# Optimization experiments

Measured on AMD Instinct MI355X. Metric: run time of the kernel, lower is better.

## Reference

```python
import jax, jax.numpy as jnp
import numpy as np

WS = 8          # window size
DIM = 192
NH = 6          # num heads
HD = DIM // NH  # head dim = 32
HIDDEN = 768    # mlp_ratio 4
EPS = 1e-5


def _rel_tables(ws):
    # continuous relative-coords table, shape (1, 2w-1, 2w-1, 2)
    r = np.arange(-(ws - 1), ws, dtype=np.float32)
    table = np.stack(np.meshgrid(r, r, indexing='ij'), axis=-1)[None]
    table = table / (ws - 1) * 8.0
    # relative position index, shape (N, N)
    coords = np.stack(np.meshgrid(np.arange(ws), np.arange(ws), indexing='ij'))
    cf = coords.reshape(2, -1)
    rel = (cf[:, :, None] - cf[:, None, :]).transpose(1, 2, 0).astype(np.int64)
    rel[:, :, 0] += ws - 1
    rel[:, :, 1] += ws - 1
    rel[:, :, 0] *= 2 * ws - 1
    idx = rel.sum(-1)
    return jnp.asarray(table), jnp.asarray(idx)

_TABLE, _RPI = _rel_tables(WS)


def _layernorm(x, g, b):
    m = jnp.mean(x, -1, keepdims=True)
    v = jnp.var(x, -1, keepdims=True)
    return (x - m) * jax.lax.rsqrt(v + EPS) * g + b


def setup_inputs() -> dict:
    key = jax.random.key(0)
    ks = jax.random.split(key, 12)
    B, H, W = 2, 256, 256
    s = 0.02
    return {
        'x': jax.random.normal(ks[0], (B, H * W, DIM), jnp.float32),
        'scale': jax.random.uniform(ks[1], (1, 2), jnp.float32, 0.5, 2.0),
        'norm1_g': jnp.ones((DIM,), jnp.float32),
        'norm1_b': jnp.zeros((DIM,), jnp.float32),
        'qkv_w': jax.random.normal(ks[2], (DIM, 3 * DIM), jnp.float32) * s,
        'qkv_b': jnp.zeros((3 * DIM,), jnp.float32),
        'proj_w': jax.random.normal(ks[3], (DIM, DIM), jnp.float32) * s,
        'proj_b': jnp.zeros((DIM,), jnp.float32),
        'cpb_w1': jax.random.normal(ks[4], (4, 512), jnp.float32) * s,
        'cpb_b1': jnp.zeros((512,), jnp.float32),
        'cpb_w2': jax.random.normal(ks[5], (512, NH), jnp.float32) * s,
        'cpb_b2': jnp.zeros((NH,), jnp.float32),
        'norm2_g': jnp.ones((DIM,), jnp.float32),
        'norm2_b': jnp.zeros((DIM,), jnp.float32),
        'fc1_w': jax.random.normal(ks[6], (DIM, HIDDEN), jnp.float32) * s,
        'fc1_b': jnp.zeros((HIDDEN,), jnp.float32),
        'fc2_w': jax.random.normal(ks[7], (HIDDEN, DIM), jnp.float32) * s,
        'fc2_b': jnp.zeros((DIM,), jnp.float32),
        'dw_w': jax.random.normal(ks[8], (HIDDEN, 1, 3, 3), jnp.float32) * s,
        'dw_b': jnp.zeros((HIDDEN,), jnp.float32),
        'H': 256,
        'W': 256,
    }


def reference(x, scale, norm1_g, norm1_b, qkv_w, qkv_b, proj_w, proj_b,
              cpb_w1, cpb_b1, cpb_w2, cpb_b2, norm2_g, norm2_b,
              fc1_w, fc1_b, fc2_w, fc2_b, dw_w, dw_b, H, W):
    B, L, C = x.shape
    N = WS * WS
    shortcut = x

    # ---- W-MSA branch ----
    h = _layernorm(x, norm1_g, norm1_b).reshape(B, H, W, C)
    # window partition -> (B*nW, N, C)
    h = h.reshape(B, H // WS, WS, W // WS, WS, C).transpose(0, 1, 3, 2, 4, 5)
    xw = h.reshape(-1, N, C)
    B_ = xw.shape[0]

    qkv = (xw @ qkv_w + qkv_b).reshape(B_, N, 3, NH, HD).transpose(2, 0, 3, 1, 4)
    q, k, v = qkv[0], qkv[1], qkv[2]          # (B_, NH, N, HD)
    q = q * (HD ** -0.5)
    attn = jnp.einsum('bhnd,bhmd->bhnm', q, k)  # (B_, NH, N, N)

    # continuous relative position bias from cpb MLP conditioned on `scale`
    rel_cell = jnp.broadcast_to(scale[:, None, None, :], _TABLE.shape)  # (1,2w-1,2w-1,2)
    coords4 = jnp.concatenate([_TABLE, rel_cell], axis=-1)              # (1,2w-1,2w-1,4)
    bias_tab = (jax.nn.relu(coords4 @ cpb_w1 + cpb_b1) @ cpb_w2 + cpb_b2).reshape(-1, NH)
    rpb = bias_tab[_RPI.reshape(-1)].reshape(N, N, NH).transpose(2, 0, 1)  # (NH,N,N)
    attn = jax.nn.softmax(attn + rpb[None], axis=-1)

    out = jnp.einsum('bhnm,bhmd->bhnd', attn, v).transpose(0, 2, 1, 3).reshape(B_, N, C)
    out = out @ proj_w + proj_b

    # window reverse
    out = out.reshape(B, H // WS, W // WS, WS, WS, C).transpose(0, 1, 3, 2, 4, 5)
    out = out.reshape(B, L, C)
    x = shortcut + out

    # ---- conv-augmented MLP branch ----
    h = _layernorm(x, norm2_g, norm2_b)
    h = jax.nn.gelu(h @ fc1_w + fc1_b, approximate=False)   # (B, L, HIDDEN)
    hc = h.transpose(0, 2, 1).reshape(B, HIDDEN, H, W)
    hc = jax.lax.conv_general_dilated(
        hc, dw_w, window_strides=(1, 1), padding=((1, 1), (1, 1)),
        dimension_numbers=('NCHW', 'OIHW', 'NCHW'), feature_group_count=HIDDEN)
    hc = hc + dw_b[None, :, None, None]
    h = hc.reshape(B, HIDDEN, L).transpose(0, 2, 1)
    h = jax.nn.gelu(h, approximate=False)
    h = h @ fc2_w + fc2_b
    return x + h
```

## Files before the change

### kernel.cpp

```cpp
#include <hip/hip_runtime.h>
#include <hip/hip_bf16.h>

typedef __attribute__((ext_vector_type(8))) short  bf16x8;
typedef __attribute__((ext_vector_type(4))) float  f32x4;
typedef __attribute__((ext_vector_type(8))) unsigned short u16x8;
typedef __attribute__((ext_vector_type(4))) unsigned short u16x4;

__device__ __forceinline__ unsigned short f2b(float f) {
    unsigned int u = __builtin_bit_cast(unsigned int, f);
    u += 0x7FFFu + ((u >> 16) & 1u);
    return (unsigned short)(u >> 16);
}
__device__ __forceinline__ float b2f(unsigned short u) {
    return __builtin_bit_cast(float, (unsigned int)u << 16);
}
__device__ __forceinline__ float gelu_fast(float x) {
    float d = 1.0f + __expf(-1.702f * x);
    return x * __builtin_amdgcn_rcpf(d);
}
__device__ __forceinline__ int wperm(int m) {
    int w = m >> 6, n = m & 63;
    int b = w >> 10, wy = (w >> 5) & 31, wx = w & 31;
    int y = wy * 8 + (n >> 3), xx = wx * 8 + (n & 7);
    return (b << 16) + (y << 8) + xx;
}

__device__ __forceinline__ void gload_lds16(const void* g, void* l) {
    __builtin_amdgcn_global_load_lds(
        (const __attribute__((address_space(1))) void*)g,
        (__attribute__((address_space(3))) void*)l, 16, 0, 0);
}

__global__ void transpose_w(const float* __restrict__ in, unsigned short* __restrict__ out,
                            int K, int N) {
    int i = blockIdx.x * 256 + threadIdx.x;
    if (i >= K * N) return;
    int n = i / K, k = i - n * K;
    out[i] = f2b(in[k * N + n]);
}

__global__ void transpose_wf(const float* __restrict__ in, float* __restrict__ out,
                             int K, int N) {
    int i = blockIdx.x * 256 + threadIdx.x;
    if (i >= K * N) return;
    int n = i / K, k = i - n * K;
    out[i] = in[k * N + n];
}

__global__ __launch_bounds__(256) void cpb_kernel(
    const float* __restrict__ scale, const float* __restrict__ w1, const float* __restrict__ b1,
    const float* __restrict__ w2, const float* __restrict__ b2, float* __restrict__ btab) {
    int t = threadIdx.x;
    if (t >= 225) return;
    int i = t / 15, j = t - (t / 15) * 15;
    float ti = (i - 7) * (8.0f / 7.0f);
    float tj = (j - 7) * (8.0f / 7.0f);
    float s0 = scale[0], s1 = scale[1];
    float acc[6];
    #pragma unroll
    for (int h = 0; h < 6; ++h) acc[h] = b2[h];
    for (int k = 0; k < 512; ++k) {
        float hv = ti * w1[k] + tj * w1[512 + k] + s0 * w1[1024 + k] + s1 * w1[1536 + k] + b1[k];
        hv = fmaxf(hv, 0.f);
        #pragma unroll
        for (int h = 0; h < 6; ++h) acc[h] += hv * w2[k * 6 + h];
    }
    #pragma unroll
    for (int h = 0; h < 6; ++h) btab[t * 6 + h] = acc[h];
}

template<int MODE>
__global__ __launch_bounds__(512) void gemm64(
    const float* __restrict__ Af,
    const float* __restrict__ lng, const float* __restrict__ lnb,
    const unsigned short* __restrict__ Bt, const float* __restrict__ bias,
    unsigned short* __restrict__ oq, unsigned short* __restrict__ ok2, unsigned short* __restrict__ ov) {
    constexpr int NCT = 3;
    __shared__ __align__(16) unsigned short Asw[3 * 64 * 64];
    __shared__ __align__(16) unsigned short Bsw[2 * 192 * 64];
    const int t = threadIdx.x, lane = t & 63, wv8 = t >> 6;
    const int wm = wv8 >> 2, wn = wv8 & 3;
    const int l15 = lane & 15, lq = lane >> 4;
    const int m0 = blockIdx.x * 64;

    int boffs[3];
    #pragma unroll
    for (int s = 0; s < 3; ++s) {
        int row = (wv8 + 8 * s) * 8 + (lane >> 3);
        boffs[s] = row * 192 + ((lane & 7) ^ (lane >> 3)) * 8;
    }
    #pragma unroll
    for (int s = 0; s < 3; ++s)
        gload_lds16(Bt + boffs[s], (char*)Bsw + (wv8 + 8 * s) * 1024);

    {
        int row = t >> 3, oct = t & 7;
        const float* p = Af + (size_t)wperm(m0 + row) * 192 + oct * 24;
        f32x4 v[6];
        float s = 0.f, q = 0.f;
        #pragma unroll
        for (int i = 0; i < 6; ++i) {
            v[i] = *(const f32x4*)(p + i * 4);
            #pragma unroll
            for (int j = 0; j < 4; ++j) { s += v[i][j]; q += v[i][j] * v[i][j]; }
        }
        s += __shfl_xor(s, 1); s += __shfl_xor(s, 2); s += __shfl_xor(s, 4);
        q += __shfl_xor(q, 1); q += __shfl_xor(q, 2); q += __shfl_xor(q, 4);
        float mean = s * (1.f / 192.f);
        float rstd = rsqrtf(q * (1.f / 192.f) - mean * mean + 1e-5f);
        #pragma unroll
        for (int i = 0; i < 6; ++i) {
            int k = oct * 24 + i * 4;
            u16x4 pk;
            #pragma unroll
            for (int j = 0; j < 4; ++j)
                pk[j] = f2b((v[i][j] - mean) * rstd * lng[k + j] + lnb[k + j]);
            int cc = k >> 6, ch = (k >> 2) & 15;
            int byte = cc * 8192 + row * 128 +
                       ((((ch >> 1) ^ (row & 7)) << 4) + ((ch & 1) << 3));
            *(u16x4*)((char*)Asw + byte) = pk;
        }
        asm volatile("s_waitcnt lgkmcnt(0)" ::: "memory");
    }

    const int axor = (l15 & 7) << 4;
    int cur = 0, it = 0;
    for (int ct = 0; ct < NCT; ++ct) {
        f32x4 acc[2][3];
        #pragma unroll
        for (int i = 0; i < 2; ++i)
            #pragma unroll
            for (int j = 0; j < 3; ++j) acc[i][j] = (f32x4){0.f, 0.f, 0.f, 0.f};
        for (int c = 0; c < 3; ++c, ++it) {
            if (it < NCT * 3 - 1) {
                int ctn = (c == 2) ? ct + 1 : ct;
                int cn  = (c == 2) ? 0 : c + 1;
                #pragma unroll
                for (int s = 0; s < 3; ++s)
                    gload_lds16(Bt + (size_t)ctn * 36864 + boffs[s] + cn * 64,
                                (char*)Bsw + (cur ^ 1) * 24576 + (wv8 + 8 * s) * 1024);
                asm volatile("s_waitcnt vmcnt(3)" ::: "memory");
            } else {
                asm volatile("s_waitcnt vmcnt(0)" ::: "memory");
            }
            __builtin_amdgcn_sched_barrier(0);
            __builtin_amdgcn_s_barrier();
            __builtin_amdgcn_sched_barrier(0);
            const char* Al = (const char*)Asw + c * 8192;
            const char* Bl = (const char*)Bsw + cur * 24576;
            #pragma unroll
            for (int kk = 0; kk < 2; ++kk) {
                bf16x8 a[2], bb[3];
                #pragma unroll
                for (int mt = 0; mt < 2; ++mt)
                    a[mt] = *(const bf16x8*)(Al + (wm * 32 + mt * 16 + l15) * 128 +
                                             ((kk << 6) ^ (lq << 4) ^ axor));
                #pragma unroll
                for (int nt = 0; nt < 3; ++nt)
                    bb[nt] = *(const bf16x8*)(Bl + (wn * 48 + nt * 16 + l15) * 128 +
                                              ((kk << 6) ^ (lq << 4) ^ axor));
                #pragma unroll
                for (int mt = 0; mt < 2; ++mt)
                    #pragma unroll
                    for (int nt = 0; nt < 3; ++nt)
                        acc[mt][nt] = __builtin_amdgcn_mfma_f32_16x16x32_bf16(a[mt], bb[nt], acc[mt][nt], 0, 0, 0);
            }
            __builtin_amdgcn_sched_barrier(0);
            __builtin_amdgcn_s_barrier();
            cur ^= 1;
        }
        unsigned short* dst = (ct == 0) ? oq : (ct == 1) ? ok2 : ov;
        float qs = (ct == 0) ? 0.17677669529663689f : 1.0f;
        #pragma unroll
        for (int mt = 0; mt < 2; ++mt)
            #pragma unroll
            for (int nt = 0; nt < 3; ++nt)
                #pragma unroll
                for (int r = 0; r < 4; ++r) {
                    int m = m0 + wm * 32 + mt * 16 + lq * 4 + r;
                    int col = wn * 48 + nt * 16 + l15;
                    float v = (acc[mt][nt][r] + bias[ct * 192 + col]) * qs;
                    int head = col >> 5, d = col & 31;
                    int w = m >> 6, n = m & 63;
                    dst[((size_t)(w * 6 + head) * 64 + n) * 32 + d] = f2b(v);
                }
    }
}

__global__ __launch_bounds__(512) void attn_proj_fc1(
    const unsigned short* __restrict__ qb, const unsigned short* __restrict__ kb,
    const unsigned short* __restrict__ vb, const float* __restrict__ btab,
    const float* __restrict__ resid,
    const unsigned short* __restrict__ projT, const float* __restrict__ projb,
    const unsigned short* __restrict__ fc1T, const float* __restrict__ fc1b,
    const float* __restrict__ n2g, const float* __restrict__ n2b,
    float* __restrict__ ofp, unsigned short* __restrict__ obf) {
    __shared__ __align__(16) unsigned short Asw[3 * 64 * 64];
    __shared__ __align__(16) unsigned short Bsw[2 * 192 * 64];
    __shared__ float scratch[1352];
    const int t = threadIdx.x, lane = t & 63, wv8 = t >> 6;
    const int wm = wv8 >> 2, wn = wv8 & 3;
    const int l15 = lane & 15, lq = lane >> 4;
    const int win = blockIdx.x;
    const int m0 = win * 64;
    const int axor = (l15 & 7) << 4;

    for (int i = t; i < 1350; i += 512) {
        int h = i / 225, idx = i - h * 225;
        scratch[i] = btab[idx * 6 + h];
    }
    __syncthreads();

    f32x4 o[4][2];
    if (wv8 < 6) {
        const size_t bid = (size_t)(win * 6 + wv8);
        const unsigned short* qp = qb + bid * 2048;
        const unsigned short* kp = kb + bid * 2048;
        const unsigned short* vp = vb + bid * 2048;
        bf16x8 qf[4], kf[4];
        #pragma unroll
        for (int i = 0; i < 4; ++i) {
            qf[i] = *(const bf16x8*)(qp + (i * 16 + l15) * 32 + lq * 8);
            kf[i] = *(const bf16x8*)(kp + (i * 16 + l15) * 32 + lq * 8);
        }
        #pragma unroll
        for (int i = 0; i < 4; ++i) {
            int c = lane + i * 64;
            int mr = c >> 2, d0 = (c & 3) * 8;
            u16x8 v = *(const u16x8*)(vp + mr * 32 + d0);
            #pragma unroll
            for (int j = 0; j < 8; ++j) {
                int row = d0 + j;
                int byte = wv8 * 4096 + row * 128 +
                           (((mr >> 3) ^ (row & 7)) << 4) + (mr & 7) * 2;
                *(unsigned short*)((char*)Asw + byte) = v[j];
            }
        }
        #pragma unroll
        for (int mt = 0; mt < 4; ++mt) {
            f32x4 s[4];
            #pragma unroll
            for (int nt = 0; nt < 4; ++nt)
                s[nt] = __builtin_amdgcn_mfma_f32_16x16x32_bf16(
                    qf[mt], kf[nt], (f32x4){0.f, 0.f, 0.f, 0.f}, 0, 0, 0);
            #pragma unroll
            for (int r = 0; r < 4; ++r) {
                int n = mt * 16 + lq * 4 + r;
                int ny = n >> 3, nx = n & 7;
                float sv[4];
                float mx = -1e30f;
                #pragma unroll
                for (int nt = 0; nt < 4; ++nt) {
                    int m = nt * 16 + l15;
                    int idx = (ny - (m >> 3) + 7) * 15 + (nx - (m & 7) + 7);
                    float val = s[nt][r] + scratch[wv8 * 225 + idx];
                    sv[nt] = val;
                    mx = fmaxf(mx, val);
                }
                #pragma unroll
                for (int off = 1; off < 16; off <<= 1) mx = fmaxf(mx, __shfl_xor(mx, off));
                float sum = 0.f;
                #pragma unroll
                for (int nt = 0; nt < 4; ++nt) { sv[nt] = __expf(sv[nt] - mx); sum += sv[nt]; }
                #pragma unroll
                for (int off = 1; off < 16; off <<= 1) sum += __shfl_xor(sum, off);
                float inv = 1.f / sum;
                #pragma unroll
                for (int nt = 0; nt < 4; ++nt) {
                    int col = nt * 16 + l15;
                    int byte = wv8 * 8192 + n * 128 +
                               (((col >> 3) ^ (n & 7)) << 4) + (col & 7) * 2;
                    *(unsigned short*)((char*)Bsw + byte) = f2b(sv[nt] * inv);
                }
            }
        }
        asm volatile("s_waitcnt lgkmcnt(0)" ::: "memory");
        #pragma unroll
        for (int i = 0; i < 4; ++i)
            #pragma unroll
            for (int j = 0; j < 2; ++j) o[i][j] = (f32x4){0.f, 0.f, 0.f, 0.f};
        #pragma unroll
        for (int mt = 0; mt < 4; ++mt)
            #pragma unroll
            for (int kk = 0; kk < 2; ++kk) {
                bf16x8 a = *(const bf16x8*)((char*)Bsw + wv8 * 8192 +
                    (mt * 16 + l15) * 128 + ((kk << 6) ^ (lq << 4) ^ axor));
                #pragma unroll
                for (int dt = 0; dt < 2; ++dt) {
                    bf16x8 b = *(const bf16x8*)((char*)Asw + wv8 * 4096 +
                        (dt * 16 + l15) * 128 + ((kk << 6) ^ (lq << 4) ^ axor));
                    o[mt][dt] = __builtin_amdgcn_mfma_f32_16x16x32_bf16(a, b, o[mt][dt], 0, 0, 0);
                }
            }
    }
    __syncthreads();
    if (wv8 < 6) {
        #pragma unroll
        for (int mt = 0; mt < 4; ++mt)
            #pragma unroll
            for (int dt = 0; dt < 2; ++dt)
                #pragma unroll
                for (int r = 0; r < 4; ++r) {
                    int row = mt * 16 + lq * 4 + r;
                    int k = wv8 * 32 + dt * 16 + l15;
                    int cc = k >> 6, k6 = k & 63;
                    int byte = cc * 8192 + row * 128 +
                               (((k6 >> 3) ^ (row & 7)) << 4) + (k6 & 7) * 2;
                    *(unsigned short*)((char*)Asw + byte) = f2b(o[mt][dt][r]);
                }
    }
    int boffs[3];
    #pragma unroll
    for (int s = 0; s < 3; ++s) {
        int row = (wv8 + 8 * s) * 8 + (lane >> 3);
        boffs[s] = row * 192 + ((lane & 7) ^ (lane >> 3)) * 8;
    }
    #pragma unroll
    for (int s = 0; s < 3; ++s)
        gload_lds16(projT + boffs[s], (char*)Bsw + (wv8 + 8 * s) * 1024);
    __syncthreads();

    int cur = 0;
    f32x4 acc[2][3];
    #pragma unroll
    for (int i = 0; i < 2; ++i)
        #pragma unroll
        for (int j = 0; j < 3; ++j) acc[i][j] = (f32x4){0.f, 0.f, 0.f, 0.f};
    for (int c = 0; c < 3; ++c) {
        if (c < 2) {
            #pragma unroll
            for (int s = 0; s < 3; ++s)
                gload_lds16(projT + boffs[s] + (c + 1) * 64,
                            (char*)Bsw + (cur ^ 1) * 24576 + (wv8 + 8 * s) * 1024);
        } else {
            #pragma unroll
            for (int s = 0; s < 3; ++s)
                gload_lds16(fc1T + boffs[s],
                            (char*)Bsw + (cur ^ 1) * 24576 + (wv8 + 8 * s) * 1024);
        }
        asm volatile("s_waitcnt vmcnt(3)" ::: "memory");
        __builtin_amdgcn_sched_barrier(0);
        __builtin_amdgcn_s_barrier();
        __builtin_amdgcn_sched_barrier(0);
        const char* Al = (const char*)Asw + c * 8192;
        const char* Bl = (const char*)Bsw + cur * 24576;
        #pragma unroll
        for (int kk = 0; kk < 2; ++kk) {
            bf16x8 a[2], bb[3];
            #pragma unroll
            for (int mt = 0; mt < 2; ++mt)
                a[mt] = *(const bf16x8*)(Al + (wm * 32 + mt * 16 + l15) * 128 +
                                         ((kk << 6) ^ (lq << 4) ^ axor));
            #pragma unroll
            for (int nt = 0; nt < 3; ++nt)
                bb[nt] = *(const bf16x8*)(Bl + (wn * 48 + nt * 16 + l15) * 128 +
                                          ((kk << 6) ^ (lq << 4) ^ axor));
            #pragma unroll
            for (int mt = 0; mt < 2; ++mt)
                #pragma unroll
                for (int nt = 0; nt < 3; ++nt)
                    acc[mt][nt] = __builtin_amdgcn_mfma_f32_16x16x32_bf16(a[mt], bb[nt], acc[mt][nt], 0, 0, 0);
        }
        __builtin_amdgcn_sched_barrier(0);
        __builtin_amdgcn_s_barrier();
        cur ^= 1;
    }
    float* sred = scratch;
    float* srow = scratch + 512;
    float hw[2][3][4];
    #pragma unroll
    for (int mt = 0; mt < 2; ++mt) {
        #pragma unroll
        for (int r = 0; r < 4; ++r) {
            int row = wm * 32 + mt * 16 + lq * 4 + r;
            int r2 = wperm(m0 + row);
            float s = 0.f, q = 0.f;
            #pragma unroll
            for (int nt = 0; nt < 3; ++nt) {
                int col = wn * 48 + nt * 16 + l15;
                size_t idx = (size_t)r2 * 192 + col;
                float wv = resid[idx] + acc[mt][nt][r] + projb[col];
                ofp[idx] = wv;
                hw[mt][nt][r] = wv;
                s += wv;
                q += wv * wv;
            }
            #pragma unroll
            for (int off = 1; off < 16; off <<= 1) {
                s += __shfl_xor(s, off);
                q += __shfl_xor(q, off);
            }
            if (l15 == 0) {
                sred[row * 8 + wn * 2]     = s;
                sred[row * 8 + wn * 2 + 1] = q;
            }
        }
    }
    __syncthreads();
    if (t < 64) {
        float s = sred[t * 8] + sred[t * 8 + 2] + sred[t * 8 + 4] + sred[t * 8 + 6];
        float q = sred[t * 8 + 1] + sred[t * 8 + 3] + sred[t * 8 + 5] + sred[t * 8 + 7];
        float mean = s * (1.f / 192.f);
        float var = q * (1.f / 192.f) - mean * mean;
        srow[t * 2] = mean;
        srow[t * 2 + 1] = rsqrtf(var + 1e-5f);
    }
    __syncthreads();
    {
        float g3[3], b3[3];
        #pragma unroll
        for (int nt = 0; nt < 3; ++nt) {
            int col = wn * 48 + nt * 16 + l15;
            g3[nt] = n2g[col];
            b3[nt] = n2b[col];
        }
        #pragma unroll
        for (int mt = 0; mt < 2; ++mt)
            #pragma unroll
            for (int r = 0; r < 4; ++r) {
                int row = wm * 32 + mt * 16 + lq * 4 + r;
                float mean = srow[row * 2], rstd = srow[row * 2 + 1];
                #pragma unroll
                for (int nt = 0; nt < 3; ++nt) {
                    int k = wn * 48 + nt * 16 + l15;
                    float nv = (hw[mt][nt][r] - mean) * rstd * g3[nt] + b3[nt];
                    int cc = k >> 6, k6 = k & 63;
                    int byte = cc * 8192 + row * 128 +
                               (((k6 >> 3) ^ (row & 7)) << 4) + (k6 & 7) * 2;
                    *(unsigned short*)((char*)Asw + byte) = f2b(nv);
                }
            }
    }
    __syncthreads();

    for (int ct = 0; ct < 4; ++ct) {
        f32x4 a2[2][3];
        #pragma unroll
        for (int i = 0; i < 2; ++i)
            #pragma unroll
            for (int j = 0; j < 3; ++j) a2[i][j] = (f32x4){0.f, 0.f, 0.f, 0.f};
        for (int c = 0; c < 3; ++c) {
            int it = ct * 3 + c;
            if (it < 11) {
                int ctn = (c == 2) ? ct + 1 : ct;
                int cn  = (c == 2) ? 0 : c + 1;
                #pragma unroll
                for (int s = 0; s < 3; ++s)
                    gload_lds16(fc1T + (size_t)ctn * 36864 + boffs[s] + cn * 64,
                                (char*)Bsw + (cur ^ 1) * 24576 + (wv8 + 8 * s) * 1024);
                asm volatile("s_waitcnt vmcnt(3)" ::: "memory");
            } else {
                asm volatile("s_waitcnt vmcnt(0)" ::: "memory");
            }
            __builtin_amdgcn_sched_barrier(0);
            __builtin_amdgcn_s_barrier();
            __builtin_amdgcn_sched_barrier(0);
            const char* Al = (const char*)Asw + c * 8192;
            const char* Bl = (const char*)Bsw + cur * 24576;
            #pragma unroll
            for (int kk = 0; kk < 2; ++kk) {
                bf16x8 a[2], bb[3];
                #pragma unroll
                for (int mt = 0; mt < 2; ++mt)
                    a[mt] = *(const bf16x8*)(Al + (wm * 32 + mt * 16 + l15) * 128 +
                                             ((kk << 6) ^ (lq << 4) ^ axor));
                #pragma unroll
                for (int nt = 0; nt < 3; ++nt)
                    bb[nt] = *(const bf16x8*)(Bl + (wn * 48 + nt * 16 + l15) * 128 +
                                              ((kk << 6) ^ (lq << 4) ^ axor));
                #pragma unroll
                for (int mt = 0; mt < 2; ++mt)
                    #pragma unroll
                    for (int nt = 0; nt < 3; ++nt)
                        a2[mt][nt] = __builtin_amdgcn_mfma_f32_16x16x32_bf16(a[mt], bb[nt], a2[mt][nt], 0, 0, 0);
            }
            __builtin_amdgcn_sched_barrier(0);
            __builtin_amdgcn_s_barrier();
            cur ^= 1;
        }
        #pragma unroll
        for (int mt = 0; mt < 2; ++mt)
            #pragma unroll
            for (int nt = 0; nt < 3; ++nt)
                #pragma unroll
                for (int r = 0; r < 4; ++r) {
                    int m = m0 + wm * 32 + mt * 16 + lq * 4 + r;
                    int col = wn * 48 + nt * 16 + l15;
                    obf[(size_t)wperm(m) * 768 + ct * 192 + col] =
                        f2b(gelu_fast(a2[mt][nt][r] + fc1b[ct * 192 + col]));
                }
    }
}

__global__ __launch_bounds__(512) void conv_fc2_v14(
    const unsigned short* __restrict__ m1, const float* __restrict__ dwwTf,
    const float* __restrict__ dwb, const unsigned short* __restrict__ fc2T,
    const float* __restrict__ fc2b, float* __restrict__ out) {
    __shared__ __align__(16) unsigned short Xs[26 * 512];
    __shared__ __align__(16) unsigned short As[128 * 72];
    __shared__ __align__(16) unsigned short Bsw[192 * 64];
    const int t = threadIdx.x;
    const int g = ((blockIdx.x & 7) << 7) + (blockIdx.x >> 3);
    const int b = g >> 9, yt = (g >> 3) & 63, xq = g & 7;
    const int y0 = yt * 4, x0 = xq * 32;
    const int cg = t & 7, lx = t >> 3;
    const int xx = lx & 31, yy0 = lx >> 5;
    const size_t ibase = (size_t)b * 65536;

    const int lane = t & 63, wv8 = t >> 6;
    const int wm = wv8 >> 1, wn = wv8 & 1;
    const int l15 = lane & 15, lq = lane >> 4;

    int xoff[4];
    #pragma unroll
    for (int s = 0; s < 4; ++s) {
        int seg = wv8 + 8 * s;
        int e = seg * 512 + lane * 8;
        e = min(e, 13048);
        int row = e / 2176;
        int rem = e - row * 2176;
        int px = rem >> 6, ch = rem & 63;
        int gy = min(max(y0 - 1 + row, 0), 255);
        int gx = min(max(x0 - 1 + px, 0), 255);
        xoff[s] = ((b << 16) + (gy << 8) + gx) * 768 + ch;
    }
    int boff[3];
    #pragma unroll
    for (int s = 0; s < 3; ++s) {
        int row = (wv8 + 8 * s) * 8 + (lane >> 3);
        boff[s] = row * 768 + ((lane & 7) ^ (lane >> 3)) * 8;
    }

    f32x4 acc[2][6];
    #pragma unroll
    for (int i = 0; i < 2; ++i)
        #pragma unroll
        for (int j = 0; j < 6; ++j) acc[i][j] = (f32x4){0.f, 0.f, 0.f, 0.f};

    #pragma unroll
    for (int s = 0; s < 4; ++s)
        if (wv8 + 8 * s < 26)
            gload_lds16(m1 + xoff[s], (char*)Xs + (wv8 + 8 * s) * 1024);
    #pragma unroll
    for (int s = 0; s < 3; ++s)
        gload_lds16(fc2T + boff[s], (char*)Bsw + (wv8 + 8 * s) * 1024);

    const int xb = xx * 128 + cg * 16;
    const int gxp = x0 + xx;
    const bool xok0 = gxp >= 1;
    const bool xok2 = gxp <= 254;
    const int oy0 = y0 + yy0;
    const int o00 = (lq * 16) ^ ((l15 & 7) << 4);
    const int brow = (wn * 96 + l15) * 128;

    for (int k0 = 0; k0 < 768; k0 += 64) {
        const int c0 = k0 + cg * 8;
        asm volatile("s_waitcnt vmcnt(0)" ::: "memory");
        __syncthreads();
        float a0[8], a1[8];
        #pragma unroll
        for (int j = 0; j < 8; ++j) { a0[j] = 0.f; a1[j] = 0.f; }
        #pragma unroll
        for (int kx = 0; kx < 3; ++kx) {
            if (kx == 0 && !xok0) continue;
            if (kx == 2 && !xok2) continue;
            #pragma unroll
            for (int ky = 0; ky < 3; ++ky) {
                const float* wp = dwwTf + (ky * 3 + kx) * 768 + c0;
                f32x4 w0 = *(const f32x4*)wp;
                f32x4 w1 = *(const f32x4*)(wp + 4);
                if ((unsigned)(oy0 + ky - 1) < 256u) {
                    u16x8 in = *(const u16x8*)((const char*)Xs +
                        (yy0 + ky) * 4352 + xb + kx * 128);
                    #pragma unroll
                    for (int j = 0; j < 4; ++j) {
                        a0[j]     += b2f(in[j]) * w0[j];
                        a0[4 + j] += b2f(in[4 + j]) * w1[j];
                    }
                }
                if ((unsigned)(oy0 + ky + 1) < 256u) {
                    u16x8 in = *(const u16x8*)((const char*)Xs +
                        (yy0 + 2 + ky) * 4352 + xb + kx * 128);
                    #pragma unroll
                    for (int j = 0; j < 4; ++j) {
                        a1[j]     += b2f(in[j]) * w0[j];
                        a1[4 + j] += b2f(in[4 + j]) * w1[j];
                    }
                }
            }
        }
        {
            f32x4 b0 = *(const f32x4*)(dwb + c0);
            f32x4 b1 = *(const f32x4*)(dwb + c0 + 4);
            u16x8 o0, o1;
            #pragma unroll
            for (int j = 0; j < 4; ++j) {
                o0[j]     = f2b(gelu_fast(a0[j] + b0[j]));
                o0[4 + j] = f2b(gelu_fast(a0[4 + j] + b1[j]));
                o1[j]     = f2b(gelu_fast(a1[j] + b0[j]));
                o1[4 + j] = f2b(gelu_fast(a1[4 + j] + b1[j]));
            }
            *(u16x8*)&As[lx * 72 + cg * 8] = o0;
            *(u16x8*)&As[(lx + 64) * 72 + cg * 8] = o1;
        }
        __syncthreads();
        if (k0 < 704) {
            #pragma unroll
            for (int s = 0; s < 4; ++s)
                if (wv8 + 8 * s < 26)
                    gload_lds16(m1 + xoff[s] + k0 + 64,
                                (char*)Xs + (wv8 + 8 * s) * 1024);
        }
        #pragma unroll
        for (int kk = 0; kk < 2; ++kk) {
            bf16x8 af[2];
            #pragma unroll
            for (int mt = 0; mt < 2; ++mt)
                af[mt] = *(bf16x8*)&As[(wm * 32 + mt * 16 + l15) * 72 + kk * 32 + lq * 8];
            #pragma unroll
            for (int nt = 0; nt < 6; ++nt) {
                bf16x8 bb = *(const bf16x8*)((const char*)Bsw + brow + nt * 2048 + (o00 ^ (kk << 6)));
                #pragma unroll
                for (int mt = 0; mt < 2; ++mt)
                    acc[mt][nt] = __builtin_amdgcn_mfma_f32_16x16x32_bf16(af[mt], bb, acc[mt][nt], 0, 0, 0);
            }
        }
        __syncthreads();
        if (k0 < 704) {
            #pragma unroll
            for (int s = 0; s < 3; ++s)
                gload_lds16(fc2T + boff[s] + k0 + 64, (char*)Bsw + (wv8 + 8 * s) * 1024);
        }
    }
    #pragma unroll
    for (int mt = 0; mt < 2; ++mt)
        #pragma unroll
        for (int nt = 0; nt < 6; ++nt)
            #pragma unroll
            for (int r = 0; r < 4; ++r) {
                int ml = wm * 32 + mt * 16 + lq * 4 + r;
                int py = ml >> 5, lxx = ml & 31;
                int col = wn * 96 + nt * 16 + l15;
                size_t idx = (ibase + (size_t)(y0 + py) * 256 + x0 + lxx) * 192 + col;
                out[idx] = out[idx] + acc[mt][nt][r] + fc2b[col];
            }
}

extern "C" void kernel_launch(void* const* d_in, const int* in_sizes, int n_in,
                              void* d_out, int out_size, void* d_ws, size_t ws_size,
                              hipStream_t stream) {
    (void)in_sizes; (void)n_in; (void)out_size; (void)ws_size;
    const float* x     = (const float*)d_in[0];
    const float* scale = (const float*)d_in[1];
    const float* n1g   = (const float*)d_in[2];
    const float* n1b   = (const float*)d_in[3];
    const float* qkvw  = (const float*)d_in[4];
    const float* qkvb  = (const float*)d_in[5];
    const float* projw = (const float*)d_in[6];
    const float* projb = (const float*)d_in[7];
    const float* cw1   = (const float*)d_in[8];
    const float* cb1   = (const float*)d_in[9];
    const float* cw2   = (const float*)d_in[10];
    const float* cb2   = (const float*)d_in[11];
    const float* n2g   = (const float*)d_in[12];
    const float* n2b   = (const float*)d_in[13];
    const float* fc1w  = (const float*)d_in[14];
    const float* fc1b  = (const float*)d_in[15];
    const float* fc2w  = (const float*)d_in[16];
    const float* fc2b  = (const float*)d_in[17];
    const float* dww   = (const float*)d_in[18];
    const float* dwb   = (const float*)d_in[19];
    float* out = (float*)d_out;

    char* ws = (char*)d_ws;
    unsigned short* qkvT  = (unsigned short*)ws;
    unsigned short* projT = qkvT + 110592;
    unsigned short* fc1T  = projT + 36864;
    unsigned short* fc2T  = fc1T + 147456;
    float* btab   = (float*)(ws + 1048576);
    float* dwwTf  = (float*)(ws + 1310720);
    unsigned short* pool = (unsigned short*)(ws + 4194304);
    const size_t S = 25165824;
    unsigned short* qb = pool;
    unsigned short* kb = pool + S;
    unsigned short* vb = pool + 2 * S;
    unsigned short* m1 = pool + 3 * S;

    transpose_w<<<432, 256, 0, stream>>>(qkvw, qkvT, 192, 576);
    transpose_w<<<144, 256, 0, stream>>>(projw, projT, 192, 192);
    transpose_w<<<576, 256, 0, stream>>>(fc1w, fc1T, 192, 768);
    transpose_w<<<576, 256, 0, stream>>>(fc2w, fc2T, 768, 192);
    transpose_wf<<<27, 256, 0, stream>>>(dww, dwwTf, 768, 9);
    cpb_kernel<<<1, 256, 0, stream>>>(scale, cw1, cb1, cw2, cb2, btab);

    gemm64<0><<<2048, 512, 0, stream>>>(x, n1g, n1b, qkvT, qkvb, qb, kb, vb);
    attn_proj_fc1<<<2048, 512, 0, stream>>>(
        qb, kb, vb, btab, x, projT, projb, fc1T, fc1b, n2g, n2b, out, m1);
    conv_fc2_v14<<<1024, 512, 0, stream>>>(m1, dwwTf, dwb, fc2T, fc2b, out);
}
```

Before: 553.2 us.

## Merge prep kernels into one launch and spread attention over all eight waves

Six small weight-transpose and CPB-table kernels are merged into a single launch that branches on block index, which removes per-launch overhead. In the attention stage, work is split into 24 (head, m-tile) units spread over all 8 waves instead of using only 6 waves with 4 m-tiles each, so the two idle waves now take a share. This adds an extra block-wide barrier between softmax and the PV product, and K fragments are reloaded for each unit.

```diff
diff --git a/kernel.cpp b/kernel.cpp
--- a/kernel.cpp
+++ b/kernel.cpp
@@ -31,42 +31,57 @@
         (__attribute__((address_space(3))) void*)l, 16, 0, 0);
 }
 
-__global__ void transpose_w(const float* __restrict__ in, unsigned short* __restrict__ out,
-                            int K, int N) {
-    int i = blockIdx.x * 256 + threadIdx.x;
-    if (i >= K * N) return;
-    int n = i / K, k = i - n * K;
-    out[i] = f2b(in[k * N + n]);
-}
-
-__global__ void transpose_wf(const float* __restrict__ in, float* __restrict__ out,
-                             int K, int N) {
-    int i = blockIdx.x * 256 + threadIdx.x;
-    if (i >= K * N) return;
-    int n = i / K, k = i - n * K;
-    out[i] = in[k * N + n];
-}
-
-__global__ __launch_bounds__(256) void cpb_kernel(
-    const float* __restrict__ scale, const float* __restrict__ w1, const float* __restrict__ b1,
-    const float* __restrict__ w2, const float* __restrict__ b2, float* __restrict__ btab) {
-    int t = threadIdx.x;
-    if (t >= 225) return;
-    int i = t / 15, j = t - (t / 15) * 15;
-    float ti = (i - 7) * (8.0f / 7.0f);
-    float tj = (j - 7) * (8.0f / 7.0f);
-    float s0 = scale[0], s1 = scale[1];
-    float acc[6];
-    #pragma unroll
-    for (int h = 0; h < 6; ++h) acc[h] = b2[h];
-    for (int k = 0; k < 512; ++k) {
-        float hv = ti * w1[k] + tj * w1[512 + k] + s0 * w1[1024 + k] + s1 * w1[1536 + k] + b1[k];
-        hv = fmaxf(hv, 0.f);
-        #pragma unroll
-        for (int h = 0; h < 6; ++h) acc[h] += hv * w2[k * 6 + h];
-    }
-    #pragma unroll
-    for (int h = 0; h < 6; ++h) btab[t * 6 + h] = acc[h];
+__global__ __launch_bounds__(256) void prep_all(
+    const float* __restrict__ qkvw, const float* __restrict__ projw,
+    const float* __restrict__ fc1w, const float* __restrict__ fc2w,
+    const float* __restrict__ dww,
+    unsigned short* __restrict__ qkvT, unsigned short* __restrict__ projT,
+    unsigned short* __restrict__ fc1T, unsigned short* __restrict__ fc2T,
+    float* __restrict__ dwwTf,
+    const float* __restrict__ scale, const float* __restrict__ w1,
+    const float* __restrict__ b1, const float* __restrict__ w2,
+    const float* __restrict__ b2, float* __restrict__ btab) {
+    const int bid = blockIdx.x, t = threadIdx.x;
+    if (bid < 432) {
+        int i = bid * 256 + t;
+        int n = i / 192, k = i - n * 192;
+        qkvT[i] = f2b(qkvw[k * 576 + n]);
+    } else if (bid < 576) {
+        int i = (bid - 432) * 256 + t;
+        int n = i / 192, k = i - n * 192;
+        projT[i] = f2b(projw[k * 192 + n]);
+    } else if (bid < 1152) {
+        int i = (bid - 576) * 256 + t;
+        int n = i / 192, k = i - n * 192;
+        fc1T[i] = f2b(fc1w[k * 768 + n]);
+    } else if (bid < 1728) {
+        int i = (bid - 1152) * 256 + t;
+        int n = i / 768, k = i - n * 768;
+        fc2T[i] = f2b(fc2w[k * 192 + n]);
+    } else if (bid < 1755) {
+        int i = (bid - 1728) * 256 + t;
+        if (i < 6912) {
+            int n = i / 768, k = i - n * 768;
+            dwwTf[i] = dww[k * 9 + n];
+        }
+    } else {
+        if (t >= 225) return;
+        int i = t / 15, j = t - (t / 15) * 15;
+        float ti = (i - 7) * (8.0f / 7.0f);
+        float tj = (j - 7) * (8.0f / 7.0f);
+        float s0 = scale[0], s1 = scale[1];
+        float acc[6];
+        #pragma unroll
+        for (int h = 0; h < 6; ++h) acc[h] = b2[h];
+        for (int k = 0; k < 512; ++k) {
+            float hv = ti * w1[k] + tj * w1[512 + k] + s0 * w1[1024 + k] + s1 * w1[1536 + k] + b1[k];
+            hv = fmaxf(hv, 0.f);
+            #pragma unroll
+            for (int h = 0; h < 6; ++h) acc[h] += hv * w2[k * 6 + h];
+        }
+        #pragma unroll
+        for (int h = 0; h < 6; ++h) btab[t * 6 + h] = acc[h];
+    }
 }
 
 template<int MODE>
@@ -204,6 +219,7 @@
     const int win = blockIdx.x;
     const int m0 = win * 64;
     const int axor = (l15 & 7) << 4;
+    const size_t wbase = (size_t)win * 6;
 
     for (int i = t; i < 1350; i += 512) {
         int h = i / 225, idx = i - h * 225;
@@ -211,103 +227,105 @@
     }
     __syncthreads();
 
-    f32x4 o[4][2];
-    if (wv8 < 6) {
-        const size_t bid = (size_t)(win * 6 + wv8);
-        const unsigned short* qp = qb + bid * 2048;
-        const unsigned short* kp = kb + bid * 2048;
-        const unsigned short* vp = vb + bid * 2048;
-        bf16x8 qf[4], kf[4];
-        #pragma unroll
-        for (int i = 0; i < 4; ++i) {
-            qf[i] = *(const bf16x8*)(qp + (i * 16 + l15) * 32 + lq * 8);
-            kf[i] = *(const bf16x8*)(kp + (i * 16 + l15) * 32 + lq * 8);
-        }
-        #pragma unroll
-        for (int i = 0; i < 4; ++i) {
-            int c = lane + i * 64;
-            int mr = c >> 2, d0 = (c & 3) * 8;
-            u16x8 v = *(const u16x8*)(vp + mr * 32 + d0);
-            #pragma unroll
-            for (int j = 0; j < 8; ++j) {
-                int row = d0 + j;
-                int byte = wv8 * 4096 + row * 128 +
-                           (((mr >> 3) ^ (row & 7)) << 4) + (mr & 7) * 2;
-                *(unsigned short*)((char*)Asw + byte) = v[j];
-            }
-        }
-        #pragma unroll
-        for (int mt = 0; mt < 4; ++mt) {
-            f32x4 s[4];
-            #pragma unroll
-            for (int nt = 0; nt < 4; ++nt)
-                s[nt] = __builtin_amdgcn_mfma_f32_16x16x32_bf16(
-                    qf[mt], kf[nt], (f32x4){0.f, 0.f, 0.f, 0.f}, 0, 0, 0);
+    #pragma unroll
+    for (int s = 0; s < 3; ++s) {
+        int u = wv8 + 8 * s;
+        int h = u >> 2;
+        const unsigned short* vp = vb + (wbase + h) * 2048;
+        int c = lane + (u & 3) * 64;
+        int mr = c >> 2, d0 = (c & 3) * 8;
+        u16x8 v = *(const u16x8*)(vp + mr * 32 + d0);
+        #pragma unroll
+        for (int j = 0; j < 8; ++j) {
+            int row = d0 + j;
+            int byte = h * 4096 + row * 128 +
+                       (((mr >> 3) ^ (row & 7)) << 4) + (mr & 7) * 2;
+            *(unsigned short*)((char*)Asw + byte) = v[j];
+        }
+    }
+    #pragma unroll
+    for (int s = 0; s < 3; ++s) {
+        int u = wv8 + 8 * s;
+        int h = u >> 2, mt = u & 3;
+        const unsigned short* qp = qb + (wbase + h) * 2048;
+        const unsigned short* kp = kb + (wbase + h) * 2048;
+        bf16x8 qf = *(const bf16x8*)(qp + (mt * 16 + l15) * 32 + lq * 8);
+        f32x4 sc[4];
+        #pragma unroll
+        for (int nt = 0; nt < 4; ++nt) {
+            bf16x8 kf = *(const bf16x8*)(kp + (nt * 16 + l15) * 32 + lq * 8);
+            sc[nt] = __builtin_amdgcn_mfma_f32_16x16x32_bf16(
+                qf, kf, (f32x4){0.f, 0.f, 0.f, 0.f}, 0, 0, 0);
+        }
+        #pragma unroll
+        for (int r = 0; r < 4; ++r) {
+            int n = mt * 16 + lq * 4 + r;
+            int ny = n >> 3, nx = n & 7;
+            float sv[4];
+            float mx = -1e30f;
+            #pragma unroll
+            for (int nt = 0; nt < 4; ++nt) {
+                int m = nt * 16 + l15;
+                int idx = (ny - (m >> 3) + 7) * 15 + (nx - (m & 7) + 7);
+                float val = sc[nt][r] + scratch[h * 225 + idx];
+                sv[nt] = val;
+                mx = fmaxf(mx, val);
+            }
+            #pragma unroll
+            for (int off = 1; off < 16; off <<= 1) mx = fmaxf(mx, __shfl_xor(mx, off));
+            float sum = 0.f;
+            #pragma unroll
+            for (int nt = 0; nt < 4; ++nt) { sv[nt] = __expf(sv[nt] - mx); sum += sv[nt]; }
+            #pragma unroll
+            for (int off = 1; off < 16; off <<= 1) sum += __shfl_xor(sum, off);
+            float inv = 1.f / sum;
+            #pragma unroll
+            for (int nt = 0; nt < 4; ++nt) {
+                int col = nt * 16 + l15;
+                int byte = h * 8192 + n * 128 +
+                           (((col >> 3) ^ (n & 7)) << 4) + (col & 7) * 2;
+                *(unsigned short*)((char*)Bsw + byte) = f2b(sv[nt] * inv);
+            }
+        }
+    }
+    __syncthreads();
+    f32x4 o[3][2];
+    #pragma unroll
+    for (int i = 0; i < 3; ++i)
+        #pragma unroll
+        for (int j = 0; j < 2; ++j) o[i][j] = (f32x4){0.f, 0.f, 0.f, 0.f};
+    #pragma unroll
+    for (int s = 0; s < 3; ++s) {
+        int u = wv8 + 8 * s;
+        int h = u >> 2, mt = u & 3;
+        #pragma unroll
+        for (int kk = 0; kk < 2; ++kk) {
+            bf16x8 a = *(const bf16x8*)((char*)Bsw + h * 8192 +
+                (mt * 16 + l15) * 128 + ((kk << 6) ^ (lq << 4) ^ axor));
+            #pragma unroll
+            for (int dt = 0; dt < 2; ++dt) {
+                bf16x8 b = *(const bf16x8*)((char*)Asw + h * 4096 +
+                    (dt * 16 + l15) * 128 + ((kk << 6) ^ (lq << 4) ^ axor));
+                o[s][dt] = __builtin_amdgcn_mfma_f32_16x16x32_bf16(a, b, o[s][dt], 0, 0, 0);
+            }
+        }
+    }
+    __syncthreads();
+    #pragma unroll
+    for (int s = 0; s < 3; ++s) {
+        int u = wv8 + 8 * s;
+        int h = u >> 2, mt = u & 3;
+        #pragma unroll
+        for (int dt = 0; dt < 2; ++dt)
             #pragma unroll
             for (int r = 0; r < 4; ++r) {
-                int n = mt * 16 + lq * 4 + r;
-                int ny = n >> 3, nx = n & 7;
-                float sv[4];
-                float mx = -1e30f;
-                #pragma unroll
-                for (int nt = 0; nt < 4; ++nt) {
-                    int m = nt * 16 + l15;
-                    int idx = (ny - (m >> 3) + 7) * 15 + (nx - (m & 7) + 7);
-                    float val = s[nt][r] + scratch[wv8 * 225 + idx];
-                    sv[nt] = val;
-                    mx = fmaxf(mx, val);
-                }
-                #pragma unroll
-                for (int off = 1; off < 16; off <<= 1) mx = fmaxf(mx, __shfl_xor(mx, off));
-                float sum = 0.f;
-                #pragma unroll
-                for (int nt = 0; nt < 4; ++nt) { sv[nt] = __expf(sv[nt] - mx); sum += sv[nt]; }
-                #pragma unroll
-                for (int off = 1; off < 16; off <<= 1) sum += __shfl_xor(sum, off);
-                float inv = 1.f / sum;
-                #pragma unroll
-                for (int nt = 0; nt < 4; ++nt) {
-                    int col = nt * 16 + l15;
-                    int byte = wv8 * 8192 + n * 128 +
-                               (((col >> 3) ^ (n & 7)) << 4) + (col & 7) * 2;
-                    *(unsigned short*)((char*)Bsw + byte) = f2b(sv[nt] * inv);
-                }
-            }
-        }
-        asm volatile("s_waitcnt lgkmcnt(0)" ::: "memory");
-        #pragma unroll
-        for (int i = 0; i < 4; ++i)
-            #pragma unroll
-            for (int j = 0; j < 2; ++j) o[i][j] = (f32x4){0.f, 0.f, 0.f, 0.f};
-        #pragma unroll
-        for (int mt = 0; mt < 4; ++mt)
-            #pragma unroll
-            for (int kk = 0; kk < 2; ++kk) {
-                bf16x8 a = *(const bf16x8*)((char*)Bsw + wv8 * 8192 +
-                    (mt * 16 + l15) * 128 + ((kk << 6) ^ (lq << 4) ^ axor));
-                #pragma unroll
-                for (int dt = 0; dt < 2; ++dt) {
-                    bf16x8 b = *(const bf16x8*)((char*)Asw + wv8 * 4096 +
-                        (dt * 16 + l15) * 128 + ((kk << 6) ^ (lq << 4) ^ axor));
-                    o[mt][dt] = __builtin_amdgcn_mfma_f32_16x16x32_bf16(a, b, o[mt][dt], 0, 0, 0);
-                }
-            }
-    }
-    __syncthreads();
-    if (wv8 < 6) {
-        #pragma unroll
-        for (int mt = 0; mt < 4; ++mt)
-            #pragma unroll
-            for (int dt = 0; dt < 2; ++dt)
-                #pragma unroll
-                for (int r = 0; r < 4; ++r) {
-                    int row = mt * 16 + lq * 4 + r;
-                    int k = wv8 * 32 + dt * 16 + l15;
-                    int cc = k >> 6, k6 = k & 63;
-                    int byte = cc * 8192 + row * 128 +
-                               (((k6 >> 3) ^ (row & 7)) << 4) + (k6 & 7) * 2;
-                    *(unsigned short*)((char*)Asw + byte) = f2b(o[mt][dt][r]);
-                }
+                int row = mt * 16 + lq * 4 + r;
+                int k = h * 32 + dt * 16 + l15;
+                int cc = k >> 6, k6 = k & 63;
+                int byte = cc * 8192 + row * 128 +
+                           (((k6 >> 3) ^ (row & 7)) << 4) + (k6 & 7) * 2;
+                *(unsigned short*)((char*)Asw + byte) = f2b(o[s][dt][r]);
+            }
     }
     int boffs[3];
     #pragma unroll
@@ -686,12 +704,9 @@
     unsigned short* vb = pool + 2 * S;
     unsigned short* m1 = pool + 3 * S;
 
-    transpose_w<<<432, 256, 0, stream>>>(qkvw, qkvT, 192, 576);
-    transpose_w<<<144, 256, 0, stream>>>(projw, projT, 192, 192);
-    transpose_w<<<576, 256, 0, stream>>>(fc1w, fc1T, 192, 768);
-    transpose_w<<<576, 256, 0, stream>>>(fc2w, fc2T, 768, 192);
-    transpose_wf<<<27, 256, 0, stream>>>(dww, dwwTf, 768, 9);
-    cpb_kernel<<<1, 256, 0, stream>>>(scale, cw1, cb1, cw2, cb2, btab);
+    prep_all<<<1756, 256, 0, stream>>>(
+        qkvw, projw, fc1w, fc2w, dww, qkvT, projT, fc1T, fc2T, dwwTf,
+        scale, cw1, cb1, cw2, cb2, btab);
 
     gemm64<0><<<2048, 512, 0, stream>>>(x, n1g, n1b, qkvT, qkvb, qb, kb, vb);
     attn_proj_fc1<<<2048, 512, 0, stream>>>(
```

Measured after the change: 532.5 us. 1.04x faster.
